# Kernel tuning notes

Hardware: AMD Instinct MI355X
Metric: run time of the kernel (lower is better)

Reference implementation:

```python
import jax, jax.numpy as jnp
import numpy as np

NREF, NALT, B, D, F = 131072, 32768, 4096, 128, 512
H = F // 2  # d_ffn // 2
EPS = 1e-5


def _ln(x, w, b):
    m = jnp.mean(x, axis=-1, keepdims=True)
    v = jnp.mean((x - m) ** 2, axis=-1, keepdims=True)
    return (x - m) * jax.lax.rsqrt(v + EPS) * w + b


def setup_inputs() -> dict:
    key = jax.random.key(0)
    ks = jax.random.split(key, 16)
    s = 0.02
    return {
        "ref_flat": jax.random.normal(ks[0], (NREF, D), jnp.float32),
        "alt_flat": jax.random.normal(ks[1], (NALT, D), jnp.float32),
        "ref_seg": jnp.sort(jax.random.randint(ks[2], (NREF,), 0, B)),
        "alt_seg": jnp.sort(jax.random.randint(ks[3], (NALT,), 0, B)),
        "norm1_w": jnp.ones((D,), jnp.float32),
        "norm1_b": jnp.zeros((D,), jnp.float32),
        "w1_ref": jax.random.normal(ks[4], (D, F), jnp.float32) * s,
        "b1_ref": jnp.zeros((F,), jnp.float32),
        "w1_alt": jax.random.normal(ks[5], (D, F), jnp.float32) * s,
        "b1_alt": jnp.zeros((F,), jnp.float32),
        "norm2_w": jnp.ones((H,), jnp.float32),
        "norm2_b": jnp.zeros((H,), jnp.float32),
        "alpha_ref": jnp.float32(0.01),
        "alpha_alt": jnp.float32(0.01),
        "beta_ref": jnp.float32(0.01),
        "beta_alt": jnp.float32(0.01),
        "gamma": jnp.float32(0.01),
        "ref_regularizer": 0.1 * jnp.ones((H,), jnp.float32),
        "reg_w_pre": jnp.float32(np.log(0.1)),
        "w2_ref": jax.random.normal(ks[6], (H, D), jnp.float32) * s,
        "b2_ref": jnp.zeros((D,), jnp.float32),
        "w2_alt": jax.random.normal(ks[7], (H, D), jnp.float32) * s,
        "b2_alt": jnp.zeros((D,), jnp.float32),
    }


def reference(ref_flat, alt_flat, ref_seg, alt_seg,
              norm1_w, norm1_b, w1_ref, b1_ref, w1_alt, b1_alt,
              norm2_w, norm2_b, alpha_ref, alpha_alt, beta_ref, beta_alt,
              gamma, ref_regularizer, reg_w_pre, w2_ref, b2_ref, w2_alt, b2_alt):
    # proj1 + SELU on flattened ragged reads
    zr = jax.nn.selu(_ln(ref_flat, norm1_w, norm1_b) @ w1_ref + b1_ref)   # [NREF, F]
    za = jax.nn.selu(_ln(alt_flat, norm1_w, norm1_b) @ w1_alt + b1_alt)   # [NALT, F]
    z1r, z2r = zr[:, :H], zr[:, H:]
    z1a, z2a = za[:, :H], za[:, H:]
    z2r = _ln(z2r, norm2_w, norm2_b)
    z2a = _ln(z2a, norm2_w, norm2_b)

    cnt_r = jax.ops.segment_sum(jnp.ones((NREF,), z2r.dtype), ref_seg, num_segments=B)
    cnt_a = jax.ops.segment_sum(jnp.ones((NALT,), z2a.dtype), alt_seg, num_segments=B)
    reg_w = jnp.exp(reg_w_pre) + 0.25
    # regularized mean field over each ref set
    ref_mf = (jax.ops.segment_sum(z2r, ref_seg, num_segments=B)
              + reg_w * ref_regularizer) / (cnt_r[:, None] + reg_w)       # [B, H]
    alt_mf = jax.ops.segment_sum(z2a, alt_seg, num_segments=B) \
             / jnp.maximum(cnt_a, 1.0)[:, None]                            # [B, H]

    ref_gate = z2r * alpha_ref + 1.0 + (beta_ref * ref_mf)[ref_seg]
    alt_gate = z2a * alpha_alt + 1.0 + (beta_alt * alt_mf + gamma * ref_mf)[alt_seg]

    out_r = ref_flat + (z1r * ref_gate) @ w2_ref + b2_ref
    out_a = alt_flat + (z1a * alt_gate) @ w2_alt + b2_alt
    return out_r, out_a
```

## Files before the change

kernel.cpp:

```cpp
#include <hip/hip_runtime.h>
#include <hip/hip_bf16.h>

#define NREF 131072
#define NALT 32768
#define BSEG 4096
#define D 128
#define F 512
#define H 256
#define EPS 1e-5f
#define NB_REF 4096
#define NB_ALT 1024

typedef short short8 __attribute__((ext_vector_type(8)));
typedef float f32x4 __attribute__((ext_vector_type(4)));

__device__ __forceinline__ float selu_f(float z) {
    const float sc = 1.0507009873554805f;
    const float al = 1.6732632423543772f;
    return z > 0.f ? sc * z : sc * al * (__expf(z) - 1.f);
}

__device__ __forceinline__ short f2bf(float v) {
    __bf16 b = (__bf16)v;
    return __builtin_bit_cast(short, b);
}

__device__ __forceinline__ float bf2f(short s) {
    return (float)__builtin_bit_cast(__bf16, s);
}

__global__ void prep_kernel(const float* __restrict__ w1_ref, const float* __restrict__ w1_alt,
                            const float* __restrict__ w2_ref, const float* __restrict__ w2_alt,
                            __bf16* __restrict__ w1p_r, __bf16* __restrict__ w1p_a,
                            __bf16* __restrict__ w2p_r, __bf16* __restrict__ w2p_a,
                            float* __restrict__ zbase) {
    int b = blockIdx.x;
    if (b < 768) {
        const float* w; __bf16* wp; int KT, N, idx;
        if (b < 256)      { w = w1_ref; wp = w1p_r; KT = 4; N = F; idx = b * 256 + threadIdx.x; }
        else if (b < 512) { w = w1_alt; wp = w1p_a; KT = 4; N = F; idx = (b - 256) * 256 + threadIdx.x; }
        else if (b < 640) { w = w2_ref; wp = w2p_r; KT = 8; N = D; idx = (b - 512) * 256 + threadIdx.x; }
        else              { w = w2_alt; wp = w2p_a; KT = 8; N = D; idx = (b - 640) * 256 + threadIdx.x; }
        int j = idx & 7;
        int l = (idx >> 3) & 63;
        int t = idx >> 9;
        int kt = t % KT;
        int nt = t / KT;
        int k = kt * 32 + ((l >> 4) << 3) + j;
        int n = (nt << 4) + (l & 15);
        wp[idx] = (__bf16)w[k * N + n];
    } else {
        int t = (b - 768) * 256 + threadIdx.x;
        float4 z = {0.f, 0.f, 0.f, 0.f};
        for (int i = t; i < 526336; i += 512 * 256)
            reinterpret_cast<float4*>(zbase)[i] = z;
    }
}

__global__ __launch_bounds__(256, 4)
void pass1_kernel(const float* __restrict__ xr_, const float* __restrict__ xa_,
                  const int* __restrict__ segr_, const int* __restrict__ sega_,
                  const __bf16* __restrict__ w1pr_, const __bf16* __restrict__ w1pa_,
                  const float* __restrict__ b1r_, const float* __restrict__ b1a_,
                  const float* __restrict__ n1w, const float* __restrict__ n1b,
                  const float* __restrict__ n2w, const float* __restrict__ n2b,
                  float* __restrict__ sumr_, float* __restrict__ cntr_,
                  float* __restrict__ suma_, float* __restrict__ cnta_,
                  __bf16* __restrict__ z2nr_, __bf16* __restrict__ z2na_,
                  int boff) {
    __shared__ __align__(16) __bf16 ys[32 * 128];
    __shared__ __align__(16) __bf16 z2s[32 * 256];
    __shared__ float n2w_s[H], n2b_s[H];
    __shared__ int seg_s[32];

    const int b = blockIdx.x + boff;
    const float* x; const int* seg; const __bf16* w1p; const float* b1;
    float* seg_sum; float* seg_cnt; __bf16* z2n_out; size_t row0;
    if (b < NB_REF) {
        x = xr_; seg = segr_; w1p = w1pr_; b1 = b1r_;
        seg_sum = sumr_; seg_cnt = cntr_; z2n_out = z2nr_;
        row0 = (size_t)b * 32;
    } else {
        x = xa_; seg = sega_; w1p = w1pa_; b1 = b1a_;
        seg_sum = suma_; seg_cnt = cnta_; z2n_out = z2na_;
        row0 = (size_t)(b - NB_REF) * 32;
    }

    const int tid = threadIdx.x;
    const int lane = tid & 63;
    const int wv = tid >> 6;
    const int q = lane >> 4, m0 = lane & 15;

    short8 bb[2][4];
    #pragma unroll
    for (int p = 0; p < 2; ++p)
        #pragma unroll
        for (int kt = 0; kt < 4; ++kt)
            bb[p][kt] = *reinterpret_cast<const short8*>(
                w1p + ((size_t)((16 + wv * 4 + p) * 4 + kt) * 64 + lane) * 8);
    float b1v[4];
    #pragma unroll
    for (int nt = 0; nt < 4; ++nt) b1v[nt] = b1[256 + (wv * 4 + nt) * 16 + m0];

    const int r = tid >> 3, g = tid & 7;
    float xr[16];
    #pragma unroll
    for (int i = 0; i < 4; ++i) {
        float4 t = *reinterpret_cast<const float4*>(x + (row0 + r) * D + g * 16 + i * 4);
        xr[i * 4 + 0] = t.x; xr[i * 4 + 1] = t.y; xr[i * 4 + 2] = t.z; xr[i * 4 + 3] = t.w;
    }
    float w1r[16], c1r[16];
    #pragma unroll
    for (int i = 0; i < 4; ++i) {
        float4 t = *reinterpret_cast<const float4*>(n1w + g * 16 + i * 4);
        w1r[i * 4 + 0] = t.x; w1r[i * 4 + 1] = t.y; w1r[i * 4 + 2] = t.z; w1r[i * 4 + 3] = t.w;
        float4 u = *reinterpret_cast<const float4*>(n1b + g * 16 + i * 4);
        c1r[i * 4 + 0] = u.x; c1r[i * 4 + 1] = u.y; c1r[i * 4 + 2] = u.z; c1r[i * 4 + 3] = u.w;
    }

    n2w_s[tid] = n2w[tid]; n2b_s[tid] = n2b[tid];
    if (tid < 32) seg_s[tid] = seg[row0 + tid];

    {
        float s = 0.f, ss = 0.f;
        #pragma unroll
        for (int i = 0; i < 16; ++i) { s += xr[i]; ss += xr[i] * xr[i]; }
        s += __shfl_xor(s, 1); ss += __shfl_xor(ss, 1);
        s += __shfl_xor(s, 2); ss += __shfl_xor(ss, 2);
        s += __shfl_xor(s, 4); ss += __shfl_xor(ss, 4);
        float mean = s * (1.f / 128.f);
        float var = ss * (1.f / 128.f) - mean * mean;
        float rsv = rsqrtf(var + EPS);
        const int swr = (r & 15) << 3;
        #pragma unroll
        for (int h = 0; h < 2; ++h) {
            short8 pk;
            #pragma unroll
            for (int j = 0; j < 8; ++j)
                pk[j] = f2bf((xr[h * 8 + j] - mean) * rsv * w1r[h * 8 + j] + c1r[h * 8 + j]);
            *reinterpret_cast<short8*>(&ys[r * 128 + ((g * 16 + h * 8) ^ swr)]) = pk;
        }
    }
    __syncthreads();

    {
        const int swm = (m0 & 15) << 3;
        const int ccol = q << 3;
        short8 a0[4], a1[4];
        #pragma unroll
        for (int kt = 0; kt < 4; ++kt) {
            a0[kt] = *reinterpret_cast<const short8*>(&ys[m0 * 128 + ((kt * 32 + ccol) ^ swm)]);
            a1[kt] = *reinterpret_cast<const short8*>(&ys[(m0 + 16) * 128 + ((kt * 32 + ccol) ^ swm)]);
        }
        #pragma unroll
        for (int nt = 0; nt < 4; ++nt) {
            f32x4 acc0 = {0.f, 0.f, 0.f, 0.f};
            f32x4 acc1 = {0.f, 0.f, 0.f, 0.f};
            #pragma unroll
            for (int kt = 0; kt < 4; ++kt) {
                acc0 = __builtin_amdgcn_mfma_f32_16x16x32_bf16(a0[kt], bb[nt & 1][kt], acc0, 0, 0, 0);
                acc1 = __builtin_amdgcn_mfma_f32_16x16x32_bf16(a1[kt], bb[nt & 1][kt], acc1, 0, 0, 0);
            }
            if (nt < 2) {
                #pragma unroll
                for (int kt = 0; kt < 4; ++kt)
                    bb[nt & 1][kt] = *reinterpret_cast<const short8*>(
                        w1p + ((size_t)((16 + wv * 4 + nt + 2) * 4 + kt) * 64 + lane) * 8);
            }
            int cz = (wv * 4 + nt) * 16 + m0;
            #pragma unroll
            for (int reg = 0; reg < 4; ++reg) {
                int r0 = (q << 2) + reg;
                int r1 = r0 + 16;
                z2s[r0 * 256 + (cz ^ ((r0 & 15) << 3))] = (__bf16)selu_f(acc0[reg] + b1v[nt]);
                z2s[r1 * 256 + (cz ^ ((r1 & 15) << 3))] = (__bf16)selu_f(acc1[reg] + b1v[nt]);
            }
        }
    }
    __syncthreads();

    {
        const int swr = (r & 15) << 3;
        float vb[32];
        float s2 = 0.f, q2 = 0.f;
        #pragma unroll
        for (int i = 0; i < 4; ++i) {
            short8 v = *reinterpret_cast<const short8*>(&z2s[r * 256 + ((g * 32 + i * 8) ^ swr)]);
            #pragma unroll
            for (int j = 0; j < 8; ++j) {
                float f = bf2f(v[j]);
                vb[i * 8 + j] = f; s2 += f; q2 += f * f;
            }
        }
        s2 += __shfl_xor(s2, 1); q2 += __shfl_xor(q2, 1);
        s2 += __shfl_xor(s2, 2); q2 += __shfl_xor(q2, 2);
        s2 += __shfl_xor(s2, 4); q2 += __shfl_xor(q2, 4);
        float mean2 = s2 * (1.f / 256.f);
        float var2 = q2 * (1.f / 256.f) - mean2 * mean2;
        float rs2 = rsqrtf(var2 + EPS);
        #pragma unroll
        for (int i = 0; i < 4; ++i) {
            short8 o;
            #pragma unroll
            for (int j = 0; j < 8; ++j) {
                int col = g * 32 + i * 8 + j;
                o[j] = f2bf((vb[i * 8 + j] - mean2) * rs2 * n2w_s[col] + n2b_s[col]);
            }
            *reinterpret_cast<short8*>(&z2s[r * 256 + ((g * 32 + i * 8) ^ swr)]) = o;
            *reinterpret_cast<short8*>(z2n_out + (row0 + r) * H + g * 32 + i * 8) = o;
        }
    }
    __syncthreads();

    {
        int c = tid;
        int s_cur = seg_s[0];
        float run = 0.f;
        for (int rr = 0; rr < 32; ++rr) {
            int sg = seg_s[rr];
            if (sg != s_cur) {
                atomicAdd(&seg_sum[(size_t)s_cur * H + c], run);
                run = 0.f; s_cur = sg;
            }
            run += (float)z2s[rr * 256 + (c ^ ((rr & 15) << 3))];
        }
        atomicAdd(&seg_sum[(size_t)s_cur * H + c], run);
        if (tid == 0) {
            int sc = seg_s[0]; float rl = 0.f;
            for (int rr = 0; rr < 32; ++rr) {
                if (seg_s[rr] != sc) { atomicAdd(&seg_cnt[sc], rl); rl = 0.f; sc = seg_s[rr]; }
                rl += 1.f;
            }
            atomicAdd(&seg_cnt[sc], rl);
        }
    }
}

__global__ void mf_kernel(const float* __restrict__ sum_r, const float* __restrict__ cnt_r,
                          const float* __restrict__ sum_a, const float* __restrict__ cnt_a,
                          const float* __restrict__ regz, const float* __restrict__ reg_w_pre,
                          const float* __restrict__ beta_ref, const float* __restrict__ beta_alt,
                          const float* __restrict__ gamma,
                          float* __restrict__ G_ref, float* __restrict__ G_alt) {
    int s = blockIdx.x, c = threadIdx.x;
    size_t i = (size_t)s * H + c;
    float rw = __expf(reg_w_pre[0]) + 0.25f;
    float mfr = (sum_r[i] + rw * regz[c]) / (cnt_r[s] + rw);
    float mfa = sum_a[i] / fmaxf(cnt_a[s], 1.f);
    G_ref[i] = beta_ref[0] * mfr;
    G_alt[i] = beta_alt[0] * mfa + gamma[0] * mfr;
}

__global__ __launch_bounds__(256, 4)
void pass2_kernel(const float* __restrict__ xr_, const float* __restrict__ xa_,
                  const int* __restrict__ segr_, const int* __restrict__ sega_,
                  const __bf16* __restrict__ w1pr_, const __bf16* __restrict__ w1pa_,
                  const float* __restrict__ b1r_, const float* __restrict__ b1a_,
                  const __bf16* __restrict__ w2pr_, const __bf16* __restrict__ w2pa_,
                  const float* __restrict__ b2r_, const float* __restrict__ b2a_,
                  const float* __restrict__ n1w, const float* __restrict__ n1b,
                  const float* __restrict__ alphar_, const float* __restrict__ alphaa_,
                  const float* __restrict__ Gr_, const float* __restrict__ Ga_,
                  const __bf16* __restrict__ z2nr_, const __bf16* __restrict__ z2na_,
                  float* __restrict__ out_, int boff) {
    __shared__ __align__(16) __bf16 ys[32 * 128];
    __shared__ __align__(16) __bf16 zs[32 * 256];

    const int b = blockIdx.x + boff;
    const bool isref = (b < NB_REF);
    const float* x; const int* seg; const __bf16* w1p; const float* b1;
    const __bf16* w2p; const float* b2; const float* alpha_p; const float* G;
    const __bf16* z2n; float* out; size_t row0;
    if (isref) {
        x = xr_; seg = segr_; w1p = w1pr_; b1 = b1r_; w2p = w2pr_; b2 = b2r_;
        alpha_p = alphar_; G = Gr_; z2n = z2nr_; out = out_;
        row0 = (size_t)b * 32;
    } else {
        x = xa_; seg = sega_; w1p = w1pa_; b1 = b1a_; w2p = w2pa_; b2 = b2a_;
        alpha_p = alphaa_; G = Ga_; z2n = z2na_; out = out_ + (size_t)NREF * D;
        row0 = (size_t)(b - NB_REF) * 32;
    }

    const int tid = threadIdx.x;
    const int lane = tid & 63;
    const int wv = tid >> 6;
    const int q = lane >> 4, m0 = lane & 15;
    const int r = tid >> 3, g = tid & 7;

    short8 bb[2][4];
    #pragma unroll
    for (int p = 0; p < 2; ++p)
        #pragma unroll
        for (int kt = 0; kt < 4; ++kt)
            bb[p][kt] = *reinterpret_cast<const short8*>(
                w1p + ((size_t)((wv * 4 + p) * 4 + kt) * 64 + lane) * 8);
    float b1v[4];
    #pragma unroll
    for (int nt = 0; nt < 4; ++nt) b1v[nt] = b1[(wv * 4 + nt) * 16 + m0];

    const int segi = seg[row0 + r];
    const float alpha = alpha_p[0];

    float xr[16];
    #pragma unroll
    for (int i = 0; i < 4; ++i) {
        float4 t = *reinterpret_cast<const float4*>(x + (row0 + r) * D + g * 16 + i * 4);
        xr[i * 4 + 0] = t.x; xr[i * 4 + 1] = t.y; xr[i * 4 + 2] = t.z; xr[i * 4 + 3] = t.w;
    }
    float w1r[16], c1r[16];
    #pragma unroll
    for (int i = 0; i < 4; ++i) {
        float4 t = *reinterpret_cast<const float4*>(n1w + g * 16 + i * 4);
        w1r[i * 4 + 0] = t.x; w1r[i * 4 + 1] = t.y; w1r[i * 4 + 2] = t.z; w1r[i * 4 + 3] = t.w;
        float4 u = *reinterpret_cast<const float4*>(n1b + g * 16 + i * 4);
        c1r[i * 4 + 0] = u.x; c1r[i * 4 + 1] = u.y; c1r[i * 4 + 2] = u.z; c1r[i * 4 + 3] = u.w;
    }

    {
        float s = 0.f, ss = 0.f;
        #pragma unroll
        for (int i = 0; i < 16; ++i) { s += xr[i]; ss += xr[i] * xr[i]; }
        s += __shfl_xor(s, 1); ss += __shfl_xor(ss, 1);
        s += __shfl_xor(s, 2); ss += __shfl_xor(ss, 2);
        s += __shfl_xor(s, 4); ss += __shfl_xor(ss, 4);
        float mean = s * (1.f / 128.f);
        float var = ss * (1.f / 128.f) - mean * mean;
        float rsv = rsqrtf(var + EPS);
        const int swr = (r & 15) << 3;
        #pragma unroll
        for (int h = 0; h < 2; ++h) {
            short8 pk;
            #pragma unroll
            for (int j = 0; j < 8; ++j)
                pk[j] = f2bf((xr[h * 8 + j] - mean) * rsv * w1r[h * 8 + j] + c1r[h * 8 + j]);
            *reinterpret_cast<short8*>(&ys[r * 128 + ((g * 16 + h * 8) ^ swr)]) = pk;
        }
    }
    __syncthreads();

    {
        const int swm = (m0 & 15) << 3;
        const int ccol = q << 3;
        short8 a0[4], a1[4];
        #pragma unroll
        for (int kt = 0; kt < 4; ++kt) {
            a0[kt] = *reinterpret_cast<const short8*>(&ys[m0 * 128 + ((kt * 32 + ccol) ^ swm)]);
            a1[kt] = *reinterpret_cast<const short8*>(&ys[(m0 + 16) * 128 + ((kt * 32 + ccol) ^ swm)]);
        }
        #pragma unroll
        for (int nt = 0; nt < 4; ++nt) {
            f32x4 acc0 = {0.f, 0.f, 0.f, 0.f};
            f32x4 acc1 = {0.f, 0.f, 0.f, 0.f};
            #pragma unroll
            for (int kt = 0; kt < 4; ++kt) {
                acc0 = __builtin_amdgcn_mfma_f32_16x16x32_bf16(a0[kt], bb[nt & 1][kt], acc0, 0, 0, 0);
                acc1 = __builtin_amdgcn_mfma_f32_16x16x32_bf16(a1[kt], bb[nt & 1][kt], acc1, 0, 0, 0);
            }
            if (nt < 2) {
                #pragma unroll
                for (int kt = 0; kt < 4; ++kt)
                    bb[nt & 1][kt] = *reinterpret_cast<const short8*>(
                        w1p + ((size_t)((wv * 4 + nt + 2) * 4 + kt) * 64 + lane) * 8);
            }
            int cz = (wv * 4 + nt) * 16 + m0;
            #pragma unroll
            for (int reg = 0; reg < 4; ++reg) {
                int r0 = (q << 2) + reg;
                int r1 = r0 + 16;
                zs[r0 * 256 + (cz ^ ((r0 & 15) << 3))] = (__bf16)selu_f(acc0[reg] + b1v[nt]);
                zs[r1 * 256 + (cz ^ ((r1 & 15) << 3))] = (__bf16)selu_f(acc1[reg] + b1v[nt]);
            }
        }
    }

    short8 zn[4];
    #pragma unroll
    for (int i = 0; i < 4; ++i)
        zn[i] = *reinterpret_cast<const short8*>(z2n + (row0 + r) * H + g * 32 + i * 8);
    float gvf[32];
    {
        const float* Gp = G + (size_t)segi * H + g * 32;
        #pragma unroll
        for (int i = 0; i < 8; ++i) {
            float4 t = *reinterpret_cast<const float4*>(Gp + i * 4);
            gvf[i * 4 + 0] = t.x; gvf[i * 4 + 1] = t.y; gvf[i * 4 + 2] = t.z; gvf[i * 4 + 3] = t.w;
        }
    }
    short8 b2f[2][8];
    #pragma unroll
    for (int p = 0; p < 2; ++p)
        #pragma unroll
        for (int kt = 0; kt < 8; ++kt)
            b2f[p][kt] = *reinterpret_cast<const short8*>(
                w2p + ((size_t)((wv * 2 + p) * 8 + kt) * 64 + lane) * 8);
    float b2v[2];
    #pragma unroll
    for (int p = 0; p < 2; ++p) b2v[p] = b2[(wv * 2 + p) * 16 + m0];
    __syncthreads();

    {
        const int swr = (r & 15) << 3;
        #pragma unroll
        for (int i = 0; i < 4; ++i) {
            int idx = r * 256 + ((g * 32 + i * 8) ^ swr);
            short8 v = *reinterpret_cast<const short8*>(&zs[idx]);
            short8 o;
            #pragma unroll
            for (int j = 0; j < 8; ++j) {
                float gate = bf2f(zn[i][j]) * alpha + 1.f + gvf[i * 8 + j];
                o[j] = f2bf(bf2f(v[j]) * gate);
            }
            *reinterpret_cast<short8*>(&zs[idx]) = o;
        }
    }
    float xres[16];
    #pragma unroll
    for (int p = 0; p < 2; ++p) {
        int col = (wv * 2 + p) * 16 + m0;
        #pragma unroll
        for (int reg = 0; reg < 4; ++reg) {
            int r0 = (q << 2) + reg;
            xres[p * 8 + reg]     = x[(row0 + r0) * D + col];
            xres[p * 8 + 4 + reg] = x[(row0 + r0 + 16) * D + col];
        }
    }
    __syncthreads();

    {
        const int swm = (m0 & 15) << 3;
        const int ccol = q << 3;
        f32x4 zero = {0.f, 0.f, 0.f, 0.f};
        f32x4 acc[2][2] = {{zero, zero}, {zero, zero}};
        #pragma unroll
        for (int kt = 0; kt < 8; ++kt) {
            short8 a0 = *reinterpret_cast<const short8*>(&zs[m0 * 256 + ((kt * 32 + ccol) ^ swm)]);
            short8 a1 = *reinterpret_cast<const short8*>(&zs[(m0 + 16) * 256 + ((kt * 32 + ccol) ^ swm)]);
            #pragma unroll
            for (int p = 0; p < 2; ++p) {
                acc[p][0] = __builtin_amdgcn_mfma_f32_16x16x32_bf16(a0, b2f[p][kt], acc[p][0], 0, 0, 0);
                acc[p][1] = __builtin_amdgcn_mfma_f32_16x16x32_bf16(a1, b2f[p][kt], acc[p][1], 0, 0, 0);
            }
        }
        #pragma unroll
        for (int p = 0; p < 2; ++p) {
            int col = (wv * 2 + p) * 16 + m0;
            #pragma unroll
            for (int reg = 0; reg < 4; ++reg) {
                int r0 = (q << 2) + reg;
                out[(row0 + r0) * D + col]      = acc[p][0][reg] + b2v[p] + xres[p * 8 + reg];
                out[(row0 + r0 + 16) * D + col] = acc[p][1][reg] + b2v[p] + xres[p * 8 + 4 + reg];
            }
        }
    }
}

extern "C" void kernel_launch(void* const* d_in, const int* in_sizes, int n_in,
                              void* d_out, int out_size, void* d_ws, size_t ws_size,
                              hipStream_t stream) {
    const float* ref_flat = (const float*)d_in[0];
    const float* alt_flat = (const float*)d_in[1];
    const int*   ref_seg  = (const int*)d_in[2];
    const int*   alt_seg  = (const int*)d_in[3];
    const float* norm1_w  = (const float*)d_in[4];
    const float* norm1_b  = (const float*)d_in[5];
    const float* w1_ref   = (const float*)d_in[6];
    const float* b1_ref   = (const float*)d_in[7];
    const float* w1_alt   = (const float*)d_in[8];
    const float* b1_alt   = (const float*)d_in[9];
    const float* norm2_w  = (const float*)d_in[10];
    const float* norm2_b  = (const float*)d_in[11];
    const float* alpha_ref = (const float*)d_in[12];
    const float* alpha_alt = (const float*)d_in[13];
    const float* beta_ref  = (const float*)d_in[14];
    const float* beta_alt  = (const float*)d_in[15];
    const float* gamma     = (const float*)d_in[16];
    const float* ref_regularizer = (const float*)d_in[17];
    const float* reg_w_pre = (const float*)d_in[18];
    const float* w2_ref   = (const float*)d_in[19];
    const float* b2_ref   = (const float*)d_in[20];
    const float* w2_alt   = (const float*)d_in[21];
    const float* b2_alt   = (const float*)d_in[22];

    char* ws = (char*)d_ws;
    float* sum_r = (float*)(ws);
    float* sum_a = (float*)(ws + 4194304);
    float* cnt_r = (float*)(ws + 8388608);
    float* cnt_a = (float*)(ws + 8404992);
    float* G_ref = (float*)(ws + 8421376);
    float* G_alt = (float*)(ws + 12615680);
    __bf16* w1p_r = (__bf16*)(ws + 16809984);
    __bf16* w1p_a = (__bf16*)(ws + 16941056);
    __bf16* w2p_r = (__bf16*)(ws + 17072128);
    __bf16* w2p_a = (__bf16*)(ws + 17137664);
    __bf16* z2n_r = (__bf16*)(ws + 17203200);
    __bf16* z2n_a = (__bf16*)(ws + 84312064);

    const bool merged = ws_size >= (size_t)101089280;
    if (!merged) z2n_a = z2n_r;

    prep_kernel<<<1280, 256, 0, stream>>>(w1_ref, w1_alt, w2_ref, w2_alt,
                                          w1p_r, w1p_a, w2p_r, w2p_a, (float*)ws);

    if (merged) {
        pass1_kernel<<<NB_REF + NB_ALT, 256, 0, stream>>>(
            ref_flat, alt_flat, ref_seg, alt_seg, w1p_r, w1p_a, b1_ref, b1_alt,
            norm1_w, norm1_b, norm2_w, norm2_b,
            sum_r, cnt_r, sum_a, cnt_a, z2n_r, z2n_a, 0);
        mf_kernel<<<BSEG, 256, 0, stream>>>(sum_r, cnt_r, sum_a, cnt_a,
                                            ref_regularizer, reg_w_pre,
                                            beta_ref, beta_alt, gamma, G_ref, G_alt);
        pass2_kernel<<<NB_REF + NB_ALT, 256, 0, stream>>>(
            ref_flat, alt_flat, ref_seg, alt_seg, w1p_r, w1p_a, b1_ref, b1_alt,
            w2p_r, w2p_a, b2_ref, b2_alt, norm1_w, norm1_b,
            alpha_ref, alpha_alt, G_ref, G_alt, z2n_r, z2n_a, (float*)d_out, 0);
    } else {
        pass1_kernel<<<NB_REF, 256, 0, stream>>>(
            ref_flat, alt_flat, ref_seg, alt_seg, w1p_r, w1p_a, b1_ref, b1_alt,
            norm1_w, norm1_b, norm2_w, norm2_b,
            sum_r, cnt_r, sum_a, cnt_a, z2n_r, z2n_a, 0);
        mf_kernel<<<BSEG, 256, 0, stream>>>(sum_r, cnt_r, sum_a, cnt_a,
                                            ref_regularizer, reg_w_pre,
                                            beta_ref, beta_alt, gamma, G_ref, G_alt);
        pass2_kernel<<<NB_REF, 256, 0, stream>>>(
            ref_flat, alt_flat, ref_seg, alt_seg, w1p_r, w1p_a, b1_ref, b1_alt,
            w2p_r, w2p_a, b2_ref, b2_alt, norm1_w, norm1_b,
            alpha_ref, alpha_alt, G_ref, G_alt, z2n_r, z2n_a, (float*)d_out, 0);
        pass1_kernel<<<NB_ALT, 256, 0, stream>>>(
            ref_flat, alt_flat, ref_seg, alt_seg, w1p_r, w1p_a, b1_ref, b1_alt,
            norm1_w, norm1_b, norm2_w, norm2_b,
            sum_r, cnt_r, sum_a, cnt_a, z2n_r, z2n_a, NB_REF);
        mf_kernel<<<BSEG, 256, 0, stream>>>(sum_r, cnt_r, sum_a, cnt_a,
                                            ref_regularizer, reg_w_pre,
                                            beta_ref, beta_alt, gamma, G_ref, G_alt);
        pass2_kernel<<<NB_ALT, 256, 0, stream>>>(
            ref_flat, alt_flat, ref_seg, alt_seg, w1p_r, w1p_a, b1_ref, b1_alt,
            w2p_r, w2p_a, b2_ref, b2_alt, norm1_w, norm1_b,
            alpha_ref, alpha_alt, G_ref, G_alt, z2n_r, z2n_a, (float*)d_out, NB_REF);
    }
}
```

Before: 304.1 us.

## Materialize z1 in pass1 and use slim pass2 without recomputing proj1

When the workspace is large enough, pass1 now computes all 512 columns of the first projection and writes the z1 half to global memory as bf16. A new slim pass2 kernel reads z1 and z2n, applies the gate and runs only the second projection, without recomputing LayerNorm and the first GEMM. This trades redundant compute for an extra write and read of a large intermediate buffer and more workspace. The z1 stores are uncoalesced 2-byte writes, which may add memory traffic cost.

Result: slower. 373.1 us (+22.7%).

```diff
diff --git a/kernel.cpp b/kernel.cpp
--- a/kernel.cpp
+++ b/kernel.cpp
@@ -57,6 +57,7 @@
     }
 }
 
+template<int WZ1>
 __global__ __launch_bounds__(256, 4)
 void pass1_kernel(const float* __restrict__ xr_, const float* __restrict__ xa_,
                   const int* __restrict__ segr_, const int* __restrict__ sega_,
@@ -67,6 +68,7 @@
                   float* __restrict__ sumr_, float* __restrict__ cntr_,
                   float* __restrict__ suma_, float* __restrict__ cnta_,
                   __bf16* __restrict__ z2nr_, __bf16* __restrict__ z2na_,
+                  __bf16* __restrict__ z1r_, __bf16* __restrict__ z1a_,
                   int boff) {
     __shared__ __align__(16) __bf16 ys[32 * 128];
     __shared__ __align__(16) __bf16 z2s[32 * 256];
@@ -75,14 +77,14 @@
 
     const int b = blockIdx.x + boff;
     const float* x; const int* seg; const __bf16* w1p; const float* b1;
-    float* seg_sum; float* seg_cnt; __bf16* z2n_out; size_t row0;
+    float* seg_sum; float* seg_cnt; __bf16* z2n_out; __bf16* z1_out; size_t row0;
     if (b < NB_REF) {
         x = xr_; seg = segr_; w1p = w1pr_; b1 = b1r_;
-        seg_sum = sumr_; seg_cnt = cntr_; z2n_out = z2nr_;
+        seg_sum = sumr_; seg_cnt = cntr_; z2n_out = z2nr_; z1_out = z1r_;
         row0 = (size_t)b * 32;
     } else {
         x = xa_; seg = sega_; w1p = w1pa_; b1 = b1a_;
-        seg_sum = suma_; seg_cnt = cnta_; z2n_out = z2na_;
+        seg_sum = suma_; seg_cnt = cnta_; z2n_out = z2na_; z1_out = z1a_;
         row0 = (size_t)(b - NB_REF) * 32;
     }
 
@@ -91,16 +93,19 @@
     const int wv = tid >> 6;
     const int q = lane >> 4, m0 = lane & 15;
 
+    const int NPW = WZ1 ? 8 : 4;
+    const int base_nt = WZ1 ? (wv * 8) : (16 + wv * 4);
+
     short8 bb[2][4];
     #pragma unroll
     for (int p = 0; p < 2; ++p)
         #pragma unroll
         for (int kt = 0; kt < 4; ++kt)
             bb[p][kt] = *reinterpret_cast<const short8*>(
-                w1p + ((size_t)((16 + wv * 4 + p) * 4 + kt) * 64 + lane) * 8);
-    float b1v[4];
-    #pragma unroll
-    for (int nt = 0; nt < 4; ++nt) b1v[nt] = b1[256 + (wv * 4 + nt) * 16 + m0];
+                w1p + ((size_t)((base_nt + p) * 4 + kt) * 64 + lane) * 8);
+    float b1v[8];
+    #pragma unroll
+    for (int nt = 0; nt < NPW; ++nt) b1v[nt] = b1[(base_nt + nt) * 16 + m0];
 
     const int r = tid >> 3, g = tid & 7;
     float xr[16];
@@ -153,7 +158,7 @@
             a1[kt] = *reinterpret_cast<const short8*>(&ys[(m0 + 16) * 128 + ((kt * 32 + ccol) ^ swm)]);
         }
         #pragma unroll
-        for (int nt = 0; nt < 4; ++nt) {
+        for (int nt = 0; nt < NPW; ++nt) {
             f32x4 acc0 = {0.f, 0.f, 0.f, 0.f};
             f32x4 acc1 = {0.f, 0.f, 0.f, 0.f};
             #pragma unroll
@@ -161,19 +166,30 @@
                 acc0 = __builtin_amdgcn_mfma_f32_16x16x32_bf16(a0[kt], bb[nt & 1][kt], acc0, 0, 0, 0);
                 acc1 = __builtin_amdgcn_mfma_f32_16x16x32_bf16(a1[kt], bb[nt & 1][kt], acc1, 0, 0, 0);
             }
-            if (nt < 2) {
+            if (nt + 2 < NPW) {
                 #pragma unroll
                 for (int kt = 0; kt < 4; ++kt)
                     bb[nt & 1][kt] = *reinterpret_cast<const short8*>(
-                        w1p + ((size_t)((16 + wv * 4 + nt + 2) * 4 + kt) * 64 + lane) * 8);
-            }
-            int cz = (wv * 4 + nt) * 16 + m0;
-            #pragma unroll
-            for (int reg = 0; reg < 4; ++reg) {
-                int r0 = (q << 2) + reg;
-                int r1 = r0 + 16;
-                z2s[r0 * 256 + (cz ^ ((r0 & 15) << 3))] = (__bf16)selu_f(acc0[reg] + b1v[nt]);
-                z2s[r1 * 256 + (cz ^ ((r1 & 15) << 3))] = (__bf16)selu_f(acc1[reg] + b1v[nt]);
+                        w1p + ((size_t)((base_nt + nt + 2) * 4 + kt) * 64 + lane) * 8);
+            }
+            const int nt_g = base_nt + nt;
+            if (WZ1 && nt_g < 16) {
+                int cz = nt_g * 16 + m0;
+                #pragma unroll
+                for (int reg = 0; reg < 4; ++reg) {
+                    int r0 = (q << 2) + reg;
+                    z1_out[(row0 + r0) * H + cz]      = (__bf16)selu_f(acc0[reg] + b1v[nt]);
+                    z1_out[(row0 + r0 + 16) * H + cz] = (__bf16)selu_f(acc1[reg] + b1v[nt]);
+                }
+            } else {
+                int cz = (nt_g - 16) * 16 + m0;
+                #pragma unroll
+                for (int reg = 0; reg < 4; ++reg) {
+                    int r0 = (q << 2) + reg;
+                    int r1 = r0 + 16;
+                    z2s[r0 * 256 + (cz ^ ((r0 & 15) << 3))] = (__bf16)selu_f(acc0[reg] + b1v[nt]);
+                    z2s[r1 * 256 + (cz ^ ((r1 & 15) << 3))] = (__bf16)selu_f(acc1[reg] + b1v[nt]);
+                }
             }
         }
     }
@@ -249,6 +265,123 @@
     float mfa = sum_a[i] / fmaxf(cnt_a[s], 1.f);
     G_ref[i] = beta_ref[0] * mfr;
     G_alt[i] = beta_alt[0] * mfa + gamma[0] * mfr;
+}
+
+__global__ __launch_bounds__(256, 6)
+void pass2s_kernel(const float* __restrict__ xr_, const float* __restrict__ xa_,
+                   const int* __restrict__ segr_, const int* __restrict__ sega_,
+                   const __bf16* __restrict__ w2pr_, const __bf16* __restrict__ w2pa_,
+                   const float* __restrict__ b2r_, const float* __restrict__ b2a_,
+                   const float* __restrict__ alphar_, const float* __restrict__ alphaa_,
+                   const float* __restrict__ Gr_, const float* __restrict__ Ga_,
+                   const __bf16* __restrict__ z1r_, const __bf16* __restrict__ z1a_,
+                   const __bf16* __restrict__ z2nr_, const __bf16* __restrict__ z2na_,
+                   float* __restrict__ out_, int boff) {
+    __shared__ __align__(16) __bf16 zs[32 * 256];
+
+    const int b = blockIdx.x + boff;
+    const bool isref = (b < NB_REF);
+    const float* x; const int* seg; const __bf16* w2p; const float* b2;
+    const float* alpha_p; const float* G; const __bf16* z1; const __bf16* z2n;
+    float* out; size_t row0;
+    if (isref) {
+        x = xr_; seg = segr_; w2p = w2pr_; b2 = b2r_;
+        alpha_p = alphar_; G = Gr_; z1 = z1r_; z2n = z2nr_; out = out_;
+        row0 = (size_t)b * 32;
+    } else {
+        x = xa_; seg = sega_; w2p = w2pa_; b2 = b2a_;
+        alpha_p = alphaa_; G = Ga_; z1 = z1a_; z2n = z2na_; out = out_ + (size_t)NREF * D;
+        row0 = (size_t)(b - NB_REF) * 32;
+    }
+
+    const int tid = threadIdx.x;
+    const int lane = tid & 63;
+    const int wv = tid >> 6;
+    const int q = lane >> 4, m0 = lane & 15;
+    const int r = tid >> 3, g = tid & 7;
+
+    const size_t rowg = (row0 + r) * H + g * 32;
+    short8 z1v[4], znv[4];
+    #pragma unroll
+    for (int i = 0; i < 4; ++i) {
+        z1v[i] = *reinterpret_cast<const short8*>(z1 + rowg + i * 8);
+        znv[i] = *reinterpret_cast<const short8*>(z2n + rowg + i * 8);
+    }
+    const int segi = seg[row0 + r];
+    const float alpha = alpha_p[0];
+    const float* Gp = G + (size_t)segi * H + g * 32;
+    float xres[16];
+    #pragma unroll
+    for (int p = 0; p < 2; ++p) {
+        int col = (wv * 2 + p) * 16 + m0;
+        #pragma unroll
+        for (int reg = 0; reg < 4; ++reg) {
+            int r0 = (q << 2) + reg;
+            xres[p * 8 + reg]     = x[(row0 + r0) * D + col];
+            xres[p * 8 + 4 + reg] = x[(row0 + r0 + 16) * D + col];
+        }
+    }
+    float b2v[2];
+    #pragma unroll
+    for (int p = 0; p < 2; ++p) b2v[p] = b2[(wv * 2 + p) * 16 + m0];
+
+    {
+        const int swr = (r & 15) << 3;
+        #pragma unroll
+        for (int i = 0; i < 4; ++i) {
+            float4 g0 = *reinterpret_cast<const float4*>(Gp + i * 8);
+            float4 g1 = *reinterpret_cast<const float4*>(Gp + i * 8 + 4);
+            float gv[8] = {g0.x, g0.y, g0.z, g0.w, g1.x, g1.y, g1.z, g1.w};
+            short8 o;
+            #pragma unroll
+            for (int j = 0; j < 8; ++j) {
+                float gate = bf2f(znv[i][j]) * alpha + 1.f + gv[j];
+                o[j] = f2bf(bf2f(z1v[i][j]) * gate);
+            }
+            *reinterpret_cast<short8*>(&zs[r * 256 + ((g * 32 + i * 8) ^ swr)]) = o;
+        }
+    }
+    __syncthreads();
+
+    {
+        const int swm = (m0 & 15) << 3;
+        const int ccol = q << 3;
+        short8 wf[2][2];
+        #pragma unroll
+        for (int s = 0; s < 2; ++s)
+            #pragma unroll
+            for (int p = 0; p < 2; ++p)
+                wf[s][p] = *reinterpret_cast<const short8*>(
+                    w2p + ((size_t)((wv * 2 + p) * 8 + s) * 64 + lane) * 8);
+        f32x4 zero = {0.f, 0.f, 0.f, 0.f};
+        f32x4 acc[2][2] = {{zero, zero}, {zero, zero}};
+        #pragma unroll
+        for (int kt = 0; kt < 8; ++kt) {
+            short8 a0 = *reinterpret_cast<const short8*>(&zs[m0 * 256 + ((kt * 32 + ccol) ^ swm)]);
+            short8 a1 = *reinterpret_cast<const short8*>(&zs[(m0 + 16) * 256 + ((kt * 32 + ccol) ^ swm)]);
+            #pragma unroll
+            for (int p = 0; p < 2; ++p) {
+                acc[p][0] = __builtin_amdgcn_mfma_f32_16x16x32_bf16(a0, wf[kt & 1][p], acc[p][0], 0, 0, 0);
+                acc[p][1] = __builtin_amdgcn_mfma_f32_16x16x32_bf16(a1, wf[kt & 1][p], acc[p][1], 0, 0, 0);
+            }
+            if (kt < 6) {
+                #pragma unroll
+                for (int p = 0; p < 2; ++p)
+                    wf[kt & 1][p] = *reinterpret_cast<const short8*>(
+                        w2p + ((size_t)((wv * 2 + p) * 8 + kt + 2) * 64 + lane) * 8);
+            }
+        }
+        #pragma unroll
+        for (int p = 0; p < 2; ++p) {
+            int col = (wv * 2 + p) * 16 + m0;
+            #pragma unroll
+            for (int reg = 0; reg < 4; ++reg) {
+                int r0 = (q << 2) + reg;
+                out[(row0 + r0) * D + col]      = acc[p][0][reg] + b2v[p] + xres[p * 8 + reg];
+                out[(row0 + r0 + 16) * D + col] = acc[p][1][reg] + b2v[p] + xres[p * 8 + 4 + reg];
+            }
+        }
+    }
 }
 
 __global__ __launch_bounds__(256, 4)
@@ -494,18 +627,33 @@
     __bf16* w2p_a = (__bf16*)(ws + 17137664);
     __bf16* z2n_r = (__bf16*)(ws + 17203200);
     __bf16* z2n_a = (__bf16*)(ws + 84312064);
-
+    __bf16* z1_r  = (__bf16*)(ws + 101089280);
+    __bf16* z1_a  = (__bf16*)(ws + 168198144);
+
+    const bool slim   = ws_size >= (size_t)184975360;
     const bool merged = ws_size >= (size_t)101089280;
     if (!merged) z2n_a = z2n_r;
 
     prep_kernel<<<1280, 256, 0, stream>>>(w1_ref, w1_alt, w2_ref, w2_alt,
                                           w1p_r, w1p_a, w2p_r, w2p_a, (float*)ws);
 
-    if (merged) {
-        pass1_kernel<<<NB_REF + NB_ALT, 256, 0, stream>>>(
+    if (slim) {
+        pass1_kernel<1><<<NB_REF + NB_ALT, 256, 0, stream>>>(
             ref_flat, alt_flat, ref_seg, alt_seg, w1p_r, w1p_a, b1_ref, b1_alt,
             norm1_w, norm1_b, norm2_w, norm2_b,
-            sum_r, cnt_r, sum_a, cnt_a, z2n_r, z2n_a, 0);
+            sum_r, cnt_r, sum_a, cnt_a, z2n_r, z2n_a, z1_r, z1_a, 0);
+        mf_kernel<<<BSEG, 256, 0, stream>>>(sum_r, cnt_r, sum_a, cnt_a,
+                                            ref_regularizer, reg_w_pre,
+                                            beta_ref, beta_alt, gamma, G_ref, G_alt);
+        pass2s_kernel<<<NB_REF + NB_ALT, 256, 0, stream>>>(
+            ref_flat, alt_flat, ref_seg, alt_seg, w2p_r, w2p_a, b2_ref, b2_alt,
+            alpha_ref, alpha_alt, G_ref, G_alt, z1_r, z1_a, z2n_r, z2n_a,
+            (float*)d_out, 0);
+    } else if (merged) {
+        pass1_kernel<0><<<NB_REF + NB_ALT, 256, 0, stream>>>(
+            ref_flat, alt_flat, ref_seg, alt_seg, w1p_r, w1p_a, b1_ref, b1_alt,
+            norm1_w, norm1_b, norm2_w, norm2_b,
+            sum_r, cnt_r, sum_a, cnt_a, z2n_r, z2n_a, z2n_r, z2n_a, 0);
         mf_kernel<<<BSEG, 256, 0, stream>>>(sum_r, cnt_r, sum_a, cnt_a,
                                             ref_regularizer, reg_w_pre,
                                             beta_ref, beta_alt, gamma, G_ref, G_alt);
@@ -514,10 +662,10 @@
             w2p_r, w2p_a, b2_ref, b2_alt, norm1_w, norm1_b,
             alpha_ref, alpha_alt, G_ref, G_alt, z2n_r, z2n_a, (float*)d_out, 0);
     } else {
-        pass1_kernel<<<NB_REF, 256, 0, stream>>>(
+        pass1_kernel<0><<<NB_REF, 256, 0, stream>>>(
             ref_flat, alt_flat, ref_seg, alt_seg, w1p_r, w1p_a, b1_ref, b1_alt,
             norm1_w, norm1_b, norm2_w, norm2_b,
-            sum_r, cnt_r, sum_a, cnt_a, z2n_r, z2n_a, 0);
+            sum_r, cnt_r, sum_a, cnt_a, z2n_r, z2n_a, z2n_r, z2n_a, 0);
         mf_kernel<<<BSEG, 256, 0, stream>>>(sum_r, cnt_r, sum_a, cnt_a,
                                             ref_regularizer, reg_w_pre,
                                             beta_ref, beta_alt, gamma, G_ref, G_alt);
@@ -525,10 +673,10 @@
             ref_flat, alt_flat, ref_seg, alt_seg, w1p_r, w1p_a, b1_ref, b1_alt,
             w2p_r, w2p_a, b2_ref, b2_alt, norm1_w, norm1_b,
             alpha_ref, alpha_alt, G_ref, G_alt, z2n_r, z2n_a, (float*)d_out, 0);
-        pass1_kernel<<<NB_ALT, 256, 0, stream>>>(
+        pass1_kernel<0><<<NB_ALT, 256, 0, stream>>>(
             ref_flat, alt_flat, ref_seg, alt_seg, w1p_r, w1p_a, b1_ref, b1_alt,
             norm1_w, norm1_b, norm2_w, norm2_b,
-            sum_r, cnt_r, sum_a, cnt_a, z2n_r, z2n_a, NB_REF);
+            sum_r, cnt_r, sum_a, cnt_a, z2n_r, z2n_a, z2n_r, z2n_a, NB_REF);
         mf_kernel<<<BSEG, 256, 0, stream>>>(sum_r, cnt_r, sum_a, cnt_a,
                                             ref_regularizer, reg_w_pre,
                                             beta_ref, beta_alt, gamma, G_ref, G_alt);
```
